# Kernel optimization log

Hardware: AMD Instinct MI355X
Metric: run time of the kernel (lower is better)

The kernel has to match this reference:

```python
import jax, jax.numpy as jnp
import numpy as np

B, S, D, H = 2, 2048, 1024, 16
HD = D // H  # head_features = 64
MASKED_BIAS = -10000.0


def setup_inputs() -> dict:
    key = jax.random.key(0)
    ks = jax.random.split(key, 5)
    return {
        "hidden_states": jax.random.normal(ks[0], (B, S, D), dtype=jnp.float32),
        "c_attn_w": jax.random.normal(ks[1], (D, 3 * D), dtype=jnp.float32) * 0.02,
        "c_attn_b": jax.random.normal(ks[2], (3 * D,), dtype=jnp.float32) * 0.02,
        "c_proj_w": jax.random.normal(ks[3], (D, D), dtype=jnp.float32) * 0.02,
        "c_proj_b": jax.random.normal(ks[4], (D,), dtype=jnp.float32) * 0.02,
    }


def reference(hidden_states, c_attn_w, c_attn_b, c_proj_w, c_proj_b):
    b, s, d = hidden_states.shape
    # Conv1D: x @ W + b, projecting D -> 3D, then split into q, k, v
    qkv = hidden_states @ c_attn_w + c_attn_b  # [b, s, 3D]
    q, k, v = jnp.split(qkv, 3, axis=-1)
    # split heads -> [b, H, s, HD]
    q = q.reshape(b, s, H, HD).transpose(0, 2, 1, 3)
    k = k.reshape(b, s, H, HD).transpose(0, 2, 1, 3)
    v = v.reshape(b, s, H, HD).transpose(0, 2, 1, 3)
    # scaled scores: [b, H, s, s]
    w = jnp.einsum("bhqd,bhkd->bhqk", q, k) / jnp.sqrt(jnp.float32(HD))
    # causal mask (tril bias buffer) applied via where with masked_bias
    causal = jnp.tril(jnp.ones((s, s), dtype=bool))
    w = jnp.where(causal[None, None], w, jnp.float32(MASKED_BIAS))
    p = jax.nn.softmax(w, axis=-1)  # attn_dropout p=0
    a = jnp.einsum("bhqk,bhkd->bhqd", p, v)  # [b, H, s, HD]
    # merge heads -> [b, s, D], output projection (resid_dropout p=0)
    a = a.transpose(0, 2, 1, 3).reshape(b, s, d)
    return a @ c_proj_w + c_proj_b
```

## Files before the change

kernel.cpp:

```cpp
#include <hip/hip_runtime.h>

typedef unsigned short u16;
typedef unsigned int   u32;

typedef __attribute__((ext_vector_type(8))) short bf16x8;
typedef __attribute__((ext_vector_type(4))) short bf16x4;
typedef __attribute__((ext_vector_type(4))) float f32x4;

typedef const __attribute__((address_space(1))) u32 gq_t;
typedef __attribute__((address_space(3))) u32 lq_t;

__device__ __forceinline__ float b2f(u16 u) {
    union { u32 u; float f; } c; c.u = ((u32)u) << 16; return c.f;
}
__device__ __forceinline__ u16 f2b(float f) {
    union { float f; u32 u; } c; c.f = f;
    u32 r = c.u + 0x7fffu + ((c.u >> 16) & 1u);
    return (u16)(r >> 16);
}

__global__ __launch_bounds__(256) void convert_x(const float* __restrict__ in,
                                                 u16* __restrict__ out) {
    const int i = (blockIdx.x * 256 + threadIdx.x) * 8;
    f32x4 a = *(const f32x4*)(in + i);
    f32x4 b = *(const f32x4*)(in + i + 4);
    union { bf16x8 v; u16 u[8]; } o;
    o.u[0] = f2b(a[0]); o.u[1] = f2b(a[1]); o.u[2] = f2b(a[2]); o.u[3] = f2b(a[3]);
    o.u[4] = f2b(b[0]); o.u[5] = f2b(b[1]); o.u[6] = f2b(b[2]); o.u[7] = f2b(b[3]);
    *(bf16x8*)(out + i) = o.v;
}

__global__ __launch_bounds__(256) void transpose_w(const float* __restrict__ in,
                                                   u16* __restrict__ out, int N) {
    __shared__ float t[32][33];
    const int k0 = blockIdx.y * 32, n0 = blockIdx.x * 32;
    const int tid = threadIdx.x;
    const int kr = tid >> 3, nc = (tid & 7) * 4;
    f32x4 v = *(const f32x4*)(in + (size_t)(k0 + kr) * N + n0 + nc);
    t[kr][nc] = v[0]; t[kr][nc + 1] = v[1]; t[kr][nc + 2] = v[2]; t[kr][nc + 3] = v[3];
    __syncthreads();
    const int nr = tid >> 3, kc = (tid & 7) * 4;
    union { bf16x4 v; u16 a[4]; } o;
    o.a[0] = f2b(t[kc][nr]);     o.a[1] = f2b(t[kc + 1][nr]);
    o.a[2] = f2b(t[kc + 2][nr]); o.a[3] = f2b(t[kc + 3][nr]);
    *(bf16x4*)(out + (size_t)(n0 + nr) * 1024 + k0 + kc) = o.v;
}

__global__ __launch_bounds__(256) void gemm128(
    const u16* __restrict__ A, const u16* __restrict__ WT,
    const float* __restrict__ bias, float* __restrict__ out,
    u16* __restrict__ Qb, u16* __restrict__ Kb, u16* __restrict__ Vt,
    int N, int K, int mode)
{
    __shared__ u16 As[128 * 32];
    __shared__ u16 Bs[128 * 32];
    const int tid  = threadIdx.x;
    const int m0   = blockIdx.y * 128, n0 = blockIdx.x * 128;
    const int wv   = tid >> 6, lane = tid & 63;
    const int wm   = (wv >> 1) * 64, wn = (wv & 1) * 64;
    const int l16  = lane & 15, quad = lane >> 4;

    const int sr = lane >> 2, sc = (lane & 3) * 8;
    const int rbase = wv * 16 + sr;

    f32x4 acc[4][4];
    const f32x4 zero = {0.f, 0.f, 0.f, 0.f};
    #pragma unroll
    for (int i = 0; i < 4; i++)
        #pragma unroll
        for (int j = 0; j < 4; j++) acc[i][j] = zero;

    for (int k0 = 0; k0 < K; k0 += 32) {
        #pragma unroll
        for (int c = 0; c < 2; c++) {
            const int rl = c * 64 + rbase;
            const u16* ag = A  + (size_t)(m0 + rl) * K + k0 + sc;
            const u16* bg = WT + (size_t)(n0 + rl) * K + k0 + sc;
            __builtin_amdgcn_global_load_lds((gq_t*)ag, (lq_t*)&As[(c * 64 + wv * 16) * 32], 16, 0, 0);
            __builtin_amdgcn_global_load_lds((gq_t*)bg, (lq_t*)&Bs[(c * 64 + wv * 16) * 32], 16, 0, 0);
        }
        __syncthreads();
        bf16x8 af[4], bf[4];
        #pragma unroll
        for (int i = 0; i < 4; i++) {
            af[i] = *(const bf16x8*)&As[(wm + i * 16 + l16) * 32 + quad * 8];
            bf[i] = *(const bf16x8*)&Bs[(wn + i * 16 + l16) * 32 + quad * 8];
        }
        #pragma unroll
        for (int i = 0; i < 4; i++)
            #pragma unroll
            for (int j = 0; j < 4; j++)
                acc[i][j] = __builtin_amdgcn_mfma_f32_16x16x32_bf16(af[i], bf[j], acc[i][j], 0, 0, 0);
        __syncthreads();
    }

    #pragma unroll
    for (int j = 0; j < 4; j++) {
        const int nn = n0 + wn + j * 16 + l16;
        const float bvf = bias[nn];
        #pragma unroll
        for (int i = 0; i < 4; i++) {
            float o[4];
            #pragma unroll
            for (int r = 0; r < 4; r++) o[r] = acc[i][j][r] + bvf;
            const int mbase = m0 + wm + i * 16 + quad * 4;
            if (mode == 0) {
                #pragma unroll
                for (int r = 0; r < 4; r++)
                    out[(size_t)(mbase + r) * N + nn] = o[r];
            } else {
                const int part = nn >> 10, w = nn & 1023;
                const int h = w >> 6, d = w & 63;
                const int b = mbase >> 11, s = mbase & 2047;
                const size_t bh = (size_t)b * 16 + h;
                if (part == 2) {
                    union { bf16x4 v; u16 a[4]; } pk;
                    #pragma unroll
                    for (int r = 0; r < 4; r++) pk.a[r] = f2b(o[r]);
                    *(bf16x4*)(Vt + (bh * 64 + d) * 2048 + s) = pk.v;
                } else {
                    u16* t = (part == 0) ? Qb : Kb;
                    const float scl = (part == 0) ? 0.125f : 1.0f;
                    #pragma unroll
                    for (int r = 0; r < 4; r++)
                        t[(bh * 2048 + s + r) * 64 + d] = f2b(o[r] * scl);
                }
            }
        }
    }
}

__global__ __launch_bounds__(256, 2) void attn_mfma(
    const u16* __restrict__ Qb, const u16* __restrict__ Kb,
    const u16* __restrict__ Vt, u16* __restrict__ Aout)
{
    const int bx   = blockIdx.x;
    const int x    = bx & 255, half = bx >> 8;
    const int slot = x >> 3;
    const int bh   = (x & 7) * 4 + (slot & 3);
    const int c8   = slot >> 2;
    const int chunk = half ? (15 - c8) : c8;
    const int q0   = chunk * 128;

    const int tid  = threadIdx.x;
    const int wave = tid >> 6, lane = tid & 63;
    const int l16  = lane & 15, quad = lane >> 4;
    const int qw   = q0 + wave * 32;
    const size_t kbase = (size_t)bh * 2048 * 64;
    const size_t vbase = (size_t)bh * 64 * 2048;

    __shared__ __align__(16) u16 Ks[2][64 * 72];
    __shared__ __align__(16) u16 Vs[2][64 * 72];
    __shared__ __align__(16) u16 p_all[4][16 * 72];
    u16* p_lds = p_all[wave];

    bf16x8 aq[2][2];
    #pragma unroll
    for (int i = 0; i < 2; i++) {
        const u16* qp = Qb + kbase + (size_t)(qw + 16 * i + l16) * 64 + quad * 8;
        aq[i][0] = *(const bf16x8*)qp;
        aq[i][1] = *(const bf16x8*)(qp + 32);
    }

    f32x4 oacc[2][4];
    const f32x4 zero = {0.f, 0.f, 0.f, 0.f};
    #pragma unroll
    for (int i = 0; i < 2; i++)
        #pragma unroll
        for (int t = 0; t < 4; t++) oacc[i][t] = zero;
    float l_[2][4] = {{0.f,0.f,0.f,0.f},{0.f,0.f,0.f,0.f}};

    const int ktlast = (qw + 31) >> 6;
    const int ktmax  = 2 * chunk + 1;

    const int srow = tid >> 2, scol = (tid & 3) * 16;
    u16* ksw0 = &Ks[0][srow * 72 + scol];
    u16* vsw0 = &Vs[0][srow * 72 + scol];
    u16* ksw1 = &Ks[1][srow * 72 + scol];
    u16* vsw1 = &Vs[1][srow * 72 + scol];

    {
        const u16* kg = Kb + kbase + (size_t)srow * 64 + scol;
        const u16* vg = Vt + vbase + (size_t)srow * 2048 + scol;
        bf16x8 k0 = *(const bf16x8*)kg, k1 = *(const bf16x8*)(kg + 8);
        bf16x8 v0 = *(const bf16x8*)vg, v1 = *(const bf16x8*)(vg + 8);
        *(bf16x8*)ksw0 = k0; *(bf16x8*)(ksw0 + 8) = k1;
        *(bf16x8*)vsw0 = v0; *(bf16x8*)(vsw0 + 8) = v1;
    }
    __syncthreads();

    for (int kt = 0; kt <= ktmax; kt++) {
        const int kb = kt * 64, buf = kt & 1;

        bf16x8 pk0, pk1, pv0, pv1;
        const bool pf = (kt < ktmax);
        if (pf) {
            const u16* kg = Kb + kbase + (size_t)(kb + 64 + srow) * 64 + scol;
            const u16* vg = Vt + vbase + (size_t)srow * 2048 + (kb + 64) + scol;
            pk0 = *(const bf16x8*)kg; pk1 = *(const bf16x8*)(kg + 8);
            pv0 = *(const bf16x8*)vg; pv1 = *(const bf16x8*)(vg + 8);
        }

        if (kt <= ktlast) {
            const u16* Kl = Ks[buf];
            const u16* Vl = Vs[buf];
            bf16x8 kk[8], vv[8];
            #pragma unroll
            for (int t = 0; t < 4; t++) {
                #pragma unroll
                for (int ks = 0; ks < 2; ks++) {
                    kk[2 * t + ks] = *(const bf16x8*)&Kl[(16 * t + l16) * 72 + ks * 32 + quad * 8];
                    vv[2 * t + ks] = *(const bf16x8*)&Vl[(16 * t + l16) * 72 + ks * 32 + quad * 8];
                }
            }
            const bool diag = (kt == ktlast);
            #pragma unroll
            for (int i = 0; i < 2; i++) {
                f32x4 sc[4];
                #pragma unroll
                for (int t = 0; t < 4; t++) {
                    sc[t] = __builtin_amdgcn_mfma_f32_16x16x32_bf16(aq[i][0], kk[2 * t],     zero,  0, 0, 0);
                    sc[t] = __builtin_amdgcn_mfma_f32_16x16x32_bf16(aq[i][1], kk[2 * t + 1], sc[t], 0, 0, 0);
                }
                #pragma unroll
                for (int r = 0; r < 4; r++) {
                    const int qi = qw + 16 * i + quad * 4 + r;
                    float p[4];
                    #pragma unroll
                    for (int t = 0; t < 4; t++) {
                        float pv = __expf(sc[t][r]);
                        if (diag && (kb + 16 * t + l16 > qi)) pv = 0.f;
                        p[t] = pv;
                    }
                    l_[i][r] += (p[0] + p[1]) + (p[2] + p[3]);
                    u16* pw = &p_lds[(quad * 4 + r) * 72 + l16];
                    pw[0]  = f2b(p[0]);
                    pw[16] = f2b(p[1]);
                    pw[32] = f2b(p[2]);
                    pw[48] = f2b(p[3]);
                }
                __asm__ volatile("s_waitcnt lgkmcnt(0)");
                #pragma unroll
                for (int ks = 0; ks < 2; ks++) {
                    bf16x8 ap = *(const bf16x8*)&p_lds[l16 * 72 + ks * 32 + quad * 8];
                    #pragma unroll
                    for (int t = 0; t < 4; t++)
                        oacc[i][t] = __builtin_amdgcn_mfma_f32_16x16x32_bf16(ap, vv[2 * t + ks], oacc[i][t], 0, 0, 0);
                }
            }
        }

        if (pf) {
            if (buf) { *(bf16x8*)ksw0 = pk0; *(bf16x8*)(ksw0 + 8) = pk1;
                       *(bf16x8*)vsw0 = pv0; *(bf16x8*)(vsw0 + 8) = pv1; }
            else     { *(bf16x8*)ksw1 = pk0; *(bf16x8*)(ksw1 + 8) = pk1;
                       *(bf16x8*)vsw1 = pv0; *(bf16x8*)(vsw1 + 8) = pv1; }
        }
        __syncthreads();
    }

    const int b = bh >> 4, h = bh & 15;
    #pragma unroll
    for (int i = 0; i < 2; i++) {
        #pragma unroll
        for (int r = 0; r < 4; r++) {
            float l = l_[i][r];
            l += __shfl_xor(l, 1);
            l += __shfl_xor(l, 2);
            l += __shfl_xor(l, 4);
            l += __shfl_xor(l, 8);
            const float inv = 1.0f / l;
            const int qi = qw + 16 * i + quad * 4 + r;
            u16* dst = Aout + (size_t)(b * 2048 + qi) * 1024 + h * 64 + l16;
            #pragma unroll
            for (int t = 0; t < 4; t++)
                dst[16 * t] = f2b(oacc[i][t][r] * inv);
        }
    }
}

extern "C" void kernel_launch(void* const* d_in, const int* in_sizes, int n_in,
                              void* d_out, int out_size, void* d_ws, size_t ws_size,
                              hipStream_t stream)
{
    const float* X    = (const float*)d_in[0];
    const float* Wqkv = (const float*)d_in[1];
    const float* Bqkv = (const float*)d_in[2];
    const float* Wp   = (const float*)d_in[3];
    const float* Bp   = (const float*)d_in[4];
    float* out = (float*)d_out;

    char* ws = (char*)d_ws;
    u16* WqkvT = (u16*)(ws);
    u16* WprojT= (u16*)(ws + 6291456);
    u16* Qb    = (u16*)(ws + 8388608);
    u16* Kb    = (u16*)(ws + 16777216);
    u16* Vt    = (u16*)(ws + 25165824);
    u16* Ab    = (u16*)(ws + 33554432);
    u16* Xb    = (u16*)(ws + 41943040);

    convert_x<<<dim3(2048), 256, 0, stream>>>(X, Xb);
    transpose_w<<<dim3(96, 32), 256, 0, stream>>>(Wqkv, WqkvT, 3072);
    transpose_w<<<dim3(32, 32), 256, 0, stream>>>(Wp, WprojT, 1024);

    gemm128<<<dim3(24, 32), 256, 0, stream>>>(Xb, WqkvT, Bqkv, nullptr,
                                              Qb, Kb, Vt, 3072, 1024, 1);
    attn_mfma<<<dim3(512), 256, 0, stream>>>(Qb, Kb, Vt, Ab);
    gemm128<<<dim3(8, 32), 256, 0, stream>>>(Ab, WprojT, Bp, out,
                                             nullptr, nullptr, nullptr, 1024, 1024, 0);
}
```

Before: 199.7 us.

## Halve attention query tile, compute row sums via MFMA, use cheaper bf16 rounding

The attention kernel now gives each block 64 query rows (16 per wave) instead of 128, doubling the grid to 1024 blocks and raising the occupancy hint to 3 blocks per CU. The intent is finer work balance and more latency hiding. The softmax denominator is now accumulated with an extra MFMA against a vector of ones instead of scalar adds plus shuffles. P is rounded to bf16 with a simpler round-half-up conversion. Each block now reloads K/V tiles for only half as many queries, which adds global and LDS traffic per unit of work.

```diff
diff --git a/kernel.cpp b/kernel.cpp
--- a/kernel.cpp
+++ b/kernel.cpp
@@ -17,6 +17,10 @@
     union { float f; u32 u; } c; c.f = f;
     u32 r = c.u + 0x7fffu + ((c.u >> 16) & 1u);
     return (u16)(r >> 16);
+}
+__device__ __forceinline__ u16 f2b_hu(float f) {
+    union { float f; u32 u; } c; c.f = f;
+    return (u16)((c.u + 0x8000u) >> 16);
 }
 
 __global__ __launch_bounds__(256) void convert_x(const float* __restrict__ in,
@@ -130,22 +134,22 @@
     }
 }
 
-__global__ __launch_bounds__(256, 2) void attn_mfma(
+__global__ __launch_bounds__(256, 3) void attn_mfma(
     const u16* __restrict__ Qb, const u16* __restrict__ Kb,
     const u16* __restrict__ Vt, u16* __restrict__ Aout)
 {
     const int bx   = blockIdx.x;
-    const int x    = bx & 255, half = bx >> 8;
-    const int slot = x >> 3;
-    const int bh   = (x & 7) * 4 + (slot & 3);
-    const int c8   = slot >> 2;
-    const int chunk = half ? (15 - c8) : c8;
-    const int q0   = chunk * 128;
+    const int x    = bx & 511, half = bx >> 9;
+    const int xcd  = x & 7, y = x >> 3;
+    const int bh   = xcd * 4 + (y & 3);
+    const int pidx = y >> 2;
+    const int chunk = half ? (31 - pidx) : pidx;
+    const int q0   = chunk * 64;
 
     const int tid  = threadIdx.x;
     const int wave = tid >> 6, lane = tid & 63;
     const int l16  = lane & 15, quad = lane >> 4;
-    const int qw   = q0 + wave * 32;
+    const int qw   = q0 + wave * 16;
     const size_t kbase = (size_t)bh * 2048 * 64;
     const size_t vbase = (size_t)bh * 64 * 2048;
 
@@ -154,24 +158,20 @@
     __shared__ __align__(16) u16 p_all[4][16 * 72];
     u16* p_lds = p_all[wave];
 
-    bf16x8 aq[2][2];
-    #pragma unroll
-    for (int i = 0; i < 2; i++) {
-        const u16* qp = Qb + kbase + (size_t)(qw + 16 * i + l16) * 64 + quad * 8;
-        aq[i][0] = *(const bf16x8*)qp;
-        aq[i][1] = *(const bf16x8*)(qp + 32);
-    }
-
-    f32x4 oacc[2][4];
+    const u16* qp = Qb + kbase + (size_t)(qw + l16) * 64 + quad * 8;
+    bf16x8 aq0 = *(const bf16x8*)qp;
+    bf16x8 aq1 = *(const bf16x8*)(qp + 32);
+
+    union { bf16x8 v; u16 a[8]; } onesu;
+    #pragma unroll
+    for (int j = 0; j < 8; j++) onesu.a[j] = 0x3F80;
+    const bf16x8 vones = onesu.v;
+
+    f32x4 oacc[4], lacc;
     const f32x4 zero = {0.f, 0.f, 0.f, 0.f};
     #pragma unroll
-    for (int i = 0; i < 2; i++)
-        #pragma unroll
-        for (int t = 0; t < 4; t++) oacc[i][t] = zero;
-    float l_[2][4] = {{0.f,0.f,0.f,0.f},{0.f,0.f,0.f,0.f}};
-
-    const int ktlast = (qw + 31) >> 6;
-    const int ktmax  = 2 * chunk + 1;
+    for (int t = 0; t < 4; t++) oacc[t] = zero;
+    lacc = zero;
 
     const int srow = tid >> 2, scol = (tid & 3) * 16;
     u16* ksw0 = &Ks[0][srow * 72 + scol];
@@ -189,11 +189,11 @@
     }
     __syncthreads();
 
-    for (int kt = 0; kt <= ktmax; kt++) {
+    for (int kt = 0; kt <= chunk; kt++) {
         const int kb = kt * 64, buf = kt & 1;
 
         bf16x8 pk0, pk1, pv0, pv1;
-        const bool pf = (kt < ktmax);
+        const bool pf = (kt < chunk);
         if (pf) {
             const u16* kg = Kb + kbase + (size_t)(kb + 64 + srow) * 64 + scol;
             const u16* vg = Vt + vbase + (size_t)srow * 2048 + (kb + 64) + scol;
@@ -201,53 +201,47 @@
             pv0 = *(const bf16x8*)vg; pv1 = *(const bf16x8*)(vg + 8);
         }
 
-        if (kt <= ktlast) {
-            const u16* Kl = Ks[buf];
-            const u16* Vl = Vs[buf];
-            bf16x8 kk[8], vv[8];
+        const u16* Kl = Ks[buf];
+        const u16* Vl = Vs[buf];
+        bf16x8 kk[8], vv[8];
+        #pragma unroll
+        for (int t = 0; t < 4; t++) {
+            #pragma unroll
+            for (int ks = 0; ks < 2; ks++) {
+                kk[2 * t + ks] = *(const bf16x8*)&Kl[(16 * t + l16) * 72 + ks * 32 + quad * 8];
+                vv[2 * t + ks] = *(const bf16x8*)&Vl[(16 * t + l16) * 72 + ks * 32 + quad * 8];
+            }
+        }
+
+        f32x4 sc[4];
+        #pragma unroll
+        for (int t = 0; t < 4; t++) {
+            sc[t] = __builtin_amdgcn_mfma_f32_16x16x32_bf16(aq0, kk[2 * t],     zero,  0, 0, 0);
+            sc[t] = __builtin_amdgcn_mfma_f32_16x16x32_bf16(aq1, kk[2 * t + 1], sc[t], 0, 0, 0);
+        }
+
+        const bool diag = (kt == chunk);
+        #pragma unroll
+        for (int r = 0; r < 4; r++) {
+            const int qi = qw + quad * 4 + r;
+            u16* pw = &p_lds[(quad * 4 + r) * 72 + l16];
             #pragma unroll
             for (int t = 0; t < 4; t++) {
-                #pragma unroll
-                for (int ks = 0; ks < 2; ks++) {
-                    kk[2 * t + ks] = *(const bf16x8*)&Kl[(16 * t + l16) * 72 + ks * 32 + quad * 8];
-                    vv[2 * t + ks] = *(const bf16x8*)&Vl[(16 * t + l16) * 72 + ks * 32 + quad * 8];
-                }
+                float pv = __expf(sc[t][r]);
+                if (diag && (kb + 16 * t + l16 > qi)) pv = 0.f;
+                pw[16 * t] = f2b_hu(pv);
             }
-            const bool diag = (kt == ktlast);
-            #pragma unroll
-            for (int i = 0; i < 2; i++) {
-                f32x4 sc[4];
-                #pragma unroll
-                for (int t = 0; t < 4; t++) {
-                    sc[t] = __builtin_amdgcn_mfma_f32_16x16x32_bf16(aq[i][0], kk[2 * t],     zero,  0, 0, 0);
-                    sc[t] = __builtin_amdgcn_mfma_f32_16x16x32_bf16(aq[i][1], kk[2 * t + 1], sc[t], 0, 0, 0);
-                }
-                #pragma unroll
-                for (int r = 0; r < 4; r++) {
-                    const int qi = qw + 16 * i + quad * 4 + r;
-                    float p[4];
-                    #pragma unroll
-                    for (int t = 0; t < 4; t++) {
-                        float pv = __expf(sc[t][r]);
-                        if (diag && (kb + 16 * t + l16 > qi)) pv = 0.f;
-                        p[t] = pv;
-                    }
-                    l_[i][r] += (p[0] + p[1]) + (p[2] + p[3]);
-                    u16* pw = &p_lds[(quad * 4 + r) * 72 + l16];
-                    pw[0]  = f2b(p[0]);
-                    pw[16] = f2b(p[1]);
-                    pw[32] = f2b(p[2]);
-                    pw[48] = f2b(p[3]);
-                }
-                __asm__ volatile("s_waitcnt lgkmcnt(0)");
-                #pragma unroll
-                for (int ks = 0; ks < 2; ks++) {
-                    bf16x8 ap = *(const bf16x8*)&p_lds[l16 * 72 + ks * 32 + quad * 8];
-                    #pragma unroll
-                    for (int t = 0; t < 4; t++)
-                        oacc[i][t] = __builtin_amdgcn_mfma_f32_16x16x32_bf16(ap, vv[2 * t + ks], oacc[i][t], 0, 0, 0);
-                }
-            }
+        }
+
+        __asm__ volatile("s_waitcnt lgkmcnt(0)");
+
+        #pragma unroll
+        for (int ks = 0; ks < 2; ks++) {
+            bf16x8 ap = *(const bf16x8*)&p_lds[l16 * 72 + ks * 32 + quad * 8];
+            #pragma unroll
+            for (int t = 0; t < 4; t++)
+                oacc[t] = __builtin_amdgcn_mfma_f32_16x16x32_bf16(ap, vv[2 * t + ks], oacc[t], 0, 0, 0);
+            lacc = __builtin_amdgcn_mfma_f32_16x16x32_bf16(ap, vones, lacc, 0, 0, 0);
         }
 
         if (pf) {
@@ -261,21 +255,13 @@
 
     const int b = bh >> 4, h = bh & 15;
     #pragma unroll
-    for (int i = 0; i < 2; i++) {
-        #pragma unroll
-        for (int r = 0; r < 4; r++) {
-            float l = l_[i][r];
-            l += __shfl_xor(l, 1);
-            l += __shfl_xor(l, 2);
-            l += __shfl_xor(l, 4);
-            l += __shfl_xor(l, 8);
-            const float inv = 1.0f / l;
-            const int qi = qw + 16 * i + quad * 4 + r;
-            u16* dst = Aout + (size_t)(b * 2048 + qi) * 1024 + h * 64 + l16;
-            #pragma unroll
-            for (int t = 0; t < 4; t++)
-                dst[16 * t] = f2b(oacc[i][t][r] * inv);
-        }
+    for (int r = 0; r < 4; r++) {
+        const float inv = 1.0f / lacc[r];
+        const int qi = qw + quad * 4 + r;
+        u16* dst = Aout + (size_t)(b * 2048 + qi) * 1024 + h * 64 + l16;
+        #pragma unroll
+        for (int t = 0; t < 4; t++)
+            dst[16 * t] = f2b(oacc[t][r] * inv);
     }
 }
 
@@ -305,7 +291,7 @@
 
     gemm128<<<dim3(24, 32), 256, 0, stream>>>(Xb, WqkvT, Bqkv, nullptr,
                                               Qb, Kb, Vt, 3072, 1024, 1);
-    attn_mfma<<<dim3(512), 256, 0, stream>>>(Qb, Kb, Vt, Ab);
+    attn_mfma<<<dim3(1024), 256, 0, stream>>>(Qb, Kb, Vt, Ab);
     gemm128<<<dim3(8, 32), 256, 0, stream>>>(Ab, WprojT, Bp, out,
                                              nullptr, nullptr, nullptr, 1024, 1024, 0);
 }
```

Result: faster. 187.8 us (-6.0%).
